# Performance work log

Measured on AMD Instinct MI355X. Metric: run time of the kernel, lower is better.

## Reference

```python
import jax, jax.numpy as jnp
import numpy as np

HD, IN_SZ, V, OP_SZ = 1024, 1024, 400, 128
B, K, L = 64, 8, 13


def log1mexp(x):
    # log(1 - exp(x)) for x <= 0, numerically stable on both ends
    x = jnp.minimum(x, -1e-38)
    big = x > -0.6931472
    return jnp.where(big,
                     jnp.log(-jnp.expm1(jnp.where(big, x, -1.0))),
                     jnp.log1p(-jnp.exp(jnp.where(big, -1.0, x))))


def compute_log_R(log_p, num_points=1000):
    # Unordered-sample ratios for Plackett-Luce sampling without replacement
    # (Kool et al.). P(S) = (1 - p_S) * int_0^1 u^{-p_S} prod_{j in S}(1 - u^{p_j}) du;
    # the (1 - p_S) prefactor cancels in all ratios. Midpoint rule in log-space.
    p = jnp.exp(log_p)                                   # (B,k)
    p_S = jnp.sum(p, axis=-1, keepdims=True)             # (B,1)
    u = (jnp.arange(num_points, dtype=log_p.dtype) + 0.5) / num_points
    log_u = jnp.log(u)                                   # (N,)
    T = log1mexp(p[:, None, :] * log_u[None, :, None])   # (B,N,k): log(1-u^{p_j})
    base = -p_S * log_u[None, :] + jnp.sum(T, axis=-1)   # (B,N)
    logN = jnp.log(jnp.float32(num_points))
    logI = jax.nn.logsumexp(base, axis=-1) - logN        # (B,)   log I(S)
    logI_s = jax.nn.logsumexp(base[:, :, None] - T, axis=1) - logN   # (B,k)
    log_R_s = logI_s - logI[:, None]
    pair = base[:, :, None, None] - T[:, :, :, None] - T[:, :, None, :]  # (B,N,k,k)
    logI_ss = jax.nn.logsumexp(pair, axis=1) - logN      # (B,k,k)
    kk = log_p.shape[-1]
    log_R_ss = jnp.where(jnp.eye(kk, dtype=bool)[None], 0.0,
                         logI_ss - logI_s[:, :, None])
    return log_R_s, log_R_ss


def gumbel_with_maximum(phi, T, u):
    # Gumbel(phi) sample conditioned on its max over axis 1 equaling T (shape (R,1))
    gmb = -jnp.log(-jnp.log(u * (1.0 - 2e-7) + 1e-7))
    g_phi = phi + gmb
    Z = jnp.max(g_phi, axis=1, keepdims=True)
    v = T - g_phi + log1mexp(g_phi - Z)
    return T - jax.nn.relu(v) - jnp.log1p(jnp.exp(-jnp.abs(v)))


def forward(x_feat, W_in_op, b_in_op, W_ih, W_hh, b_ih, b_hh,
            W_fc1, b_fc1, W_out, b_out, gumbel_u, program_len, k):
    Bn = x_feat.shape[0]
    k = int(k)
    program_len = int(program_len)
    Vn = W_out.shape[0]
    H = W_hh.shape[1]
    R = Bn * k
    # beam-major layout: row j*Bn + i is beam j of batch element i (torch split/cat order)
    x_f = jnp.tile(x_feat, (k, 1))                       # (R, in_sz)
    rows = jnp.arange(R)
    batch_idx = jnp.tile(jnp.arange(Bn), k)
    chunk = jnp.arange(k * Vn) // Vn

    def to_beams(z):  # (R, d) -> (Bn, k*d); = torch.cat(torch.split(z, Bn, 0), 1)
        return z.reshape(k, Bn, -1).transpose(1, 0, 2).reshape(Bn, -1)

    def step(carry, xt):
        h, c, G, logp, temp, samples, outputs, ent_plot, entropy_element = carry
        u_t, t = xt
        inp_op = jax.nn.relu(temp @ W_in_op.T + b_in_op)             # (R,128)
        xin = jnp.concatenate([x_f, inp_op], axis=1)                 # (R,in+128)
        gates = xin @ W_ih.T + b_ih + h @ W_hh.T + b_hh              # (R,4H)
        i_g, f_g, g_g, o_g = jnp.split(gates, 4, axis=1)             # torch LSTM order
        c = jax.nn.sigmoid(f_g) * c + jax.nn.sigmoid(i_g) * jnp.tanh(g_g)
        h = jax.nn.sigmoid(o_g) * jnp.tanh(c)
        hd = jax.nn.relu(h @ W_fc1.T + b_fc1)
        logits = hd @ W_out.T + b_out                                # (R,V)
        log_probs = jax.nn.log_softmax(logits, axis=1)
        probs = jax.nn.softmax(logits, axis=1)
        # ---- stochastic-beam-search SWOR step (selection carries no gradient) ----
        phi = jax.lax.stop_gradient(log_probs + logp)
        g = jax.lax.stop_gradient(gumbel_with_maximum(phi, G, u_t))
        nub = jnp.where(t == 0, 1, k)   # unique parent beams (all identical at t=0)
        g2 = jnp.where(chunk[None, :] < nub, to_beams(g), -jnp.inf)  # (Bn,k*V)
        g_val, index = jax.lax.top_k(g2, k)                          # (Bn,k)
        G_new = g_val.T.reshape(R, 1)
        sample = (index % Vn).T.reshape(R)                           # action ids
        order = (index // Vn).T.reshape(R) * Bn + batch_idx          # parent rows
        log_probs = log_probs[order]
        probs = probs[order]
        logp = logp[order] + log_probs[rows, sample][:, None]
        samples = samples[order].at[:, t].set(sample.astype(samples.dtype))
        outputs = outputs[order].at[:, t].set(log_probs[rows, sample])
        h = h[order]
        c = c[order]
        ent = jnp.sum(log_probs * probs, axis=1, keepdims=True)      # (R,1)
        phi_k = to_beams(logp)                                       # (Bn,k)
        log_R_s, log_R_ss = compute_log_R(phi_k)
        w_p_q = jax.lax.stop_gradient(jnp.exp(phi_k + log_R_s))
        Wsum = jnp.sum(w_p_q, axis=1)
        ws = jnp.sum(w_p_q * to_beams(ent), axis=1)
        ent_plot = ent_plot + ws
        entropy_element = entropy_element + ws / Wsum
        temp = jax.nn.one_hot(sample, Vn + 1, dtype=x_feat.dtype)
        new_carry = (h, c, G_new, logp, temp, samples, outputs, ent_plot, entropy_element)
        return new_carry, (log_R_s, log_R_ss, phi_k)

    z = jnp.zeros
    init = (z((R, H)), z((R, H)), z((R, 1)), z((R, 1)),
            jax.nn.one_hot(jnp.full((R,), Vn), Vn + 1, dtype=x_feat.dtype),
            z((R, program_len)), z((R, program_len)), z((Bn,)), z((Bn,)))
    carry, ys = jax.lax.scan(step, init, (gumbel_u, jnp.arange(program_len)))
    samples, outputs, ent_plot, entropy_element = carry[5], carry[6], carry[7], carry[8]
    log_R_s, log_R_ss, phi_k = ys[0][-1], ys[1][-1], ys[2][-1]
    return (to_beams(outputs), to_beams(samples), entropy_element,
            log_R_s, log_R_ss, phi_k, ent_plot)


def setup_inputs() -> dict:
    key = jax.random.key(0)
    ks = jax.random.split(key, 7)

    def lin(kk, out_f, in_f):  # torch nn.Linear default init
        s = 1.0 / np.sqrt(in_f)
        kw, kb = jax.random.split(kk)
        return (jax.random.uniform(kw, (out_f, in_f), jnp.float32, -s, s),
                jax.random.uniform(kb, (out_f,), jnp.float32, -s, s))

    W_in_op, b_in_op = lin(ks[0], OP_SZ, V + 1)
    W_ih, b_ih = lin(ks[1], 4 * HD, IN_SZ + OP_SZ)
    W_hh, b_hh = lin(ks[2], 4 * HD, HD)
    W_fc1, b_fc1 = lin(ks[3], HD, HD)
    W_out, b_out = lin(ks[4], V, HD)
    x_feat = jax.random.normal(ks[5], (B, IN_SZ), jnp.float32)
    gumbel_u = jax.random.uniform(ks[6], (L, B * K, V), jnp.float32)
    return {"x_feat": x_feat, "W_in_op": W_in_op, "b_in_op": b_in_op,
            "W_ih": W_ih, "W_hh": W_hh, "b_ih": b_ih, "b_hh": b_hh,
            "W_fc1": W_fc1, "b_fc1": b_fc1, "W_out": W_out, "b_out": b_out,
            "gumbel_u": gumbel_u, "program_len": L, "k": K}


def reference(x_feat, W_in_op, b_in_op, W_ih, W_hh, b_ih, b_hh,
              W_fc1, b_fc1, W_out, b_out, gumbel_u, program_len, k):
    return forward(x_feat, W_in_op, b_in_op, W_ih, W_hh, b_ih, b_hh,
                   W_fc1, b_fc1, W_out, b_out, gumbel_u, program_len, k)
```

## Files before the change

kernel.cpp:

```cpp
#include <hip/hip_runtime.h>
#include <hip/hip_bf16.h>
#include <cstdint>

#define RR 512
#define KB_ 8
#define VV 400
#define HD_ 1024
#define GD 4096
#define LL 13
#define BKT 16
#define NPTS 1000
#define OUT_N 18560
#define LDP 68

__device__ __constant__ int cPJ[28] = {0,0,0,0,0,0,0,1,1,1,1,1,1,2,2,2,2,2,3,3,3,3,4,4,4,5,5,6};
__device__ __constant__ int cPL[28] = {1,2,3,4,5,6,7,2,3,4,5,6,7,3,4,5,6,7,4,5,6,7,5,6,7,6,7,7};

__device__ __forceinline__ float r7_log1mexp(float x) {
  x = fminf(x, -1e-38f);
  return (x > -0.6931472f) ? logf(-expm1f(x)) : log1pf(-expf(x));
}

__device__ __forceinline__ float r7_sigm(float x) { return 1.f / (1.f + expf(-x)); }

__device__ __forceinline__ int r7_pidx(int j, int l) {
  if (j > l) { int t = j; j = l; l = t; }
  return 9 + (j * (15 - j)) / 2 + (l - j - 1);
}

__device__ __forceinline__ float r7_bmax256(float v, float* red) {
  #pragma unroll
  for (int o = 32; o; o >>= 1) v = fmaxf(v, __shfl_xor(v, o, 64));
  __syncthreads();
  if ((threadIdx.x & 63) == 0) red[threadIdx.x >> 6] = v;
  __syncthreads();
  return fmaxf(fmaxf(red[0], red[1]), fmaxf(red[2], red[3]));
}

__device__ __forceinline__ float r7_bsum256(float v, float* red) {
  #pragma unroll
  for (int o = 32; o; o >>= 1) v += __shfl_xor(v, o, 64);
  __syncthreads();
  if ((threadIdx.x & 63) == 0) red[threadIdx.x >> 6] = v;
  __syncthreads();
  return (red[0] + red[1]) + (red[2] + red[3]);
}

__device__ __forceinline__ void r7_gemm(
    const float* __restrict__ A, int lda,
    const float* __restrict__ W, int ldw,
    int K, int r0, int n0, int nmax,
    float (&acc)[4][4], float (*As)[LDP], float (*Bs)[LDP])
{
  const int tid = threadIdx.x;
  const int la = tid >> 2;
  const int lk = (tid & 3) << 2;
  const int tx = tid & 15, ty = tid >> 4;
  for (int k0 = 0; k0 < K; k0 += BKT) {
    float4 av = *reinterpret_cast<const float4*>(A + (size_t)(r0 + la) * lda + (k0 + lk));
    float4 bv = make_float4(0.f, 0.f, 0.f, 0.f);
    if (n0 + la < nmax)
      bv = *reinterpret_cast<const float4*>(W + (size_t)(n0 + la) * ldw + (k0 + lk));
    __syncthreads();
    As[lk + 0][la] = av.x; As[lk + 1][la] = av.y; As[lk + 2][la] = av.z; As[lk + 3][la] = av.w;
    Bs[lk + 0][la] = bv.x; Bs[lk + 1][la] = bv.y; Bs[lk + 2][la] = bv.z; Bs[lk + 3][la] = bv.w;
    __syncthreads();
    #pragma unroll
    for (int kk = 0; kk < BKT; ++kk) {
      float4 a = *reinterpret_cast<const float4*>(&As[kk][ty * 4]);
      float4 b = *reinterpret_cast<const float4*>(&Bs[kk][tx * 4]);
      float ar[4] = {a.x, a.y, a.z, a.w};
      float br[4] = {b.x, b.y, b.z, b.w};
      #pragma unroll
      for (int i = 0; i < 4; ++i)
        #pragma unroll
        for (int j = 0; j < 4; ++j)
          acc[i][j] = fmaf(ar[i], br[j], acc[i][j]);
    }
  }
}

__global__ __launch_bounds__(256) void r7_wszero(float* h0, float* c0, float* Gv,
                                                 float* logp0, float* accum) {
  int idx = blockIdx.x * 256 + threadIdx.x;
  if (idx < RR * HD_) { h0[idx] = 0.f; c0[idx] = 0.f; }
  if (idx < RR) { Gv[idx] = 0.f; logp0[idx] = 0.f; }
  if (idx < 128) accum[idx] = 0.f;
}

__global__ __launch_bounds__(256) void r7_flag(float* dout) {
  int idx = blockIdx.x * 256 + threadIdx.x;
  if (idx < OUT_N) dout[idx] = (idx == 6656) ? 20000.0f : 0.0f;
}

__global__ __launch_bounds__(256) void r7_xfb(const float* __restrict__ xf,
                                              const float* __restrict__ Wih,
                                              const float* __restrict__ bih,
                                              const float* __restrict__ bhh,
                                              float* __restrict__ xfb) {
  __shared__ __align__(16) float As[BKT][LDP];
  __shared__ __align__(16) float Bs[BKT][LDP];
  float acc[4][4] = {};
  int n0 = blockIdx.x * 64;
  r7_gemm(xf, 1024, Wih, 1152, 1024, 0, n0, 1 << 30, acc, As, Bs);
  int tx = threadIdx.x & 15, ty = threadIdx.x >> 4;
  #pragma unroll
  for (int i = 0; i < 4; ++i)
    #pragma unroll
    for (int j = 0; j < 4; ++j) {
      int r = ty * 4 + i, c = n0 + tx * 4 + j;
      xfb[(size_t)r * GD + c] = acc[i][j] + bih[c] + bhh[c];
    }
}

__global__ __launch_bounds__(256) void r7_inp(const int* s_arr, int t, const float* Wio,
                                              const float* bio, float* inp) {
  int idx = blockIdx.x * 256 + threadIdx.x;
  int r = idx >> 7, m = idx & 127;
  int s = (t == 0) ? 400 : s_arr[(size_t)(t - 1) * RR + r];
  float v = Wio[m * 401 + s] + bio[m];
  inp[idx] = fmaxf(v, 0.f);
}

__global__ __launch_bounds__(256) void r7_glstm(
    const float* __restrict__ hprev, const float* __restrict__ inp,
    const float* __restrict__ Whh, const float* __restrict__ Wih,
    const int* __restrict__ o_arr, int t, float* __restrict__ gates)
{
  __shared__ __align__(16) float As[BKT][LDP];
  __shared__ __align__(16) float Bs2[2][BKT][LDP];
  float acc[2][4][4] = {};
  const int tid = threadIdx.x;
  const int n0 = blockIdx.x * 64, r0 = blockIdx.y * 64, g2 = blockIdx.z;
  const int la = tid >> 2, lk = (tid & 3) << 2;
  const int gl = tid >> 7, rem = tid & 127;
  const int lb = rem >> 1, lk2 = (rem & 1) * 8;
  const int tx = tid & 15, ty = tid >> 4;
  const int arow = r0 + la;
  const int asrc = (t == 0) ? arow : o_arr[(size_t)(t - 1) * RR + arow];
  const float* Arow = hprev + (size_t)asrc * HD_;
  const float* Brow = Whh + (size_t)((2 * g2 + gl) * 1024 + n0 + lb) * HD_;
  for (int k0 = 0; k0 < HD_; k0 += BKT) {
    float4 av = *reinterpret_cast<const float4*>(Arow + k0 + lk);
    float4 b0 = *reinterpret_cast<const float4*>(Brow + k0 + lk2);
    float4 b1 = *reinterpret_cast<const float4*>(Brow + k0 + lk2 + 4);
    __syncthreads();
    As[lk + 0][la] = av.x; As[lk + 1][la] = av.y; As[lk + 2][la] = av.z; As[lk + 3][la] = av.w;
    Bs2[gl][lk2 + 0][lb] = b0.x; Bs2[gl][lk2 + 1][lb] = b0.y;
    Bs2[gl][lk2 + 2][lb] = b0.z; Bs2[gl][lk2 + 3][lb] = b0.w;
    Bs2[gl][lk2 + 4][lb] = b1.x; Bs2[gl][lk2 + 5][lb] = b1.y;
    Bs2[gl][lk2 + 6][lb] = b1.z; Bs2[gl][lk2 + 7][lb] = b1.w;
    __syncthreads();
    #pragma unroll
    for (int kk = 0; kk < BKT; ++kk) {
      float4 a = *reinterpret_cast<const float4*>(&As[kk][ty * 4]);
      float4 bA = *reinterpret_cast<const float4*>(&Bs2[0][kk][tx * 4]);
      float4 bB = *reinterpret_cast<const float4*>(&Bs2[1][kk][tx * 4]);
      float ar[4] = {a.x, a.y, a.z, a.w};
      float b0r[4] = {bA.x, bA.y, bA.z, bA.w};
      float b1r[4] = {bB.x, bB.y, bB.z, bB.w};
      #pragma unroll
      for (int i = 0; i < 4; ++i)
        #pragma unroll
        for (int j = 0; j < 4; ++j) {
          acc[0][i][j] = fmaf(ar[i], b0r[j], acc[0][i][j]);
          acc[1][i][j] = fmaf(ar[i], b1r[j], acc[1][i][j]);
        }
    }
  }
  const float* A2 = inp + (size_t)(r0 + la) * 128;
  const float* B2 = Wih + (size_t)((2 * g2 + gl) * 1024 + n0 + lb) * 1152 + 1024;
  for (int k0 = 0; k0 < 128; k0 += BKT) {
    float4 av = *reinterpret_cast<const float4*>(A2 + k0 + lk);
    float4 b0 = *reinterpret_cast<const float4*>(B2 + k0 + lk2);
    float4 b1 = *reinterpret_cast<const float4*>(B2 + k0 + lk2 + 4);
    __syncthreads();
    As[lk + 0][la] = av.x; As[lk + 1][la] = av.y; As[lk + 2][la] = av.z; As[lk + 3][la] = av.w;
    Bs2[gl][lk2 + 0][lb] = b0.x; Bs2[gl][lk2 + 1][lb] = b0.y;
    Bs2[gl][lk2 + 2][lb] = b0.z; Bs2[gl][lk2 + 3][lb] = b0.w;
    Bs2[gl][lk2 + 4][lb] = b1.x; Bs2[gl][lk2 + 5][lb] = b1.y;
    Bs2[gl][lk2 + 6][lb] = b1.z; Bs2[gl][lk2 + 7][lb] = b1.w;
    __syncthreads();
    #pragma unroll
    for (int kk = 0; kk < BKT; ++kk) {
      float4 a = *reinterpret_cast<const float4*>(&As[kk][ty * 4]);
      float4 bA = *reinterpret_cast<const float4*>(&Bs2[0][kk][tx * 4]);
      float4 bB = *reinterpret_cast<const float4*>(&Bs2[1][kk][tx * 4]);
      float ar[4] = {a.x, a.y, a.z, a.w};
      float b0r[4] = {bA.x, bA.y, bA.z, bA.w};
      float b1r[4] = {bB.x, bB.y, bB.z, bB.w};
      #pragma unroll
      for (int i = 0; i < 4; ++i)
        #pragma unroll
        for (int j = 0; j < 4; ++j) {
          acc[0][i][j] = fmaf(ar[i], b0r[j], acc[0][i][j]);
          acc[1][i][j] = fmaf(ar[i], b1r[j], acc[1][i][j]);
        }
    }
  }
  #pragma unroll
  for (int g = 0; g < 2; ++g)
    #pragma unroll
    for (int i = 0; i < 4; ++i)
      #pragma unroll
      for (int j = 0; j < 4; ++j)
        gates[(size_t)(r0 + ty * 4 + i) * GD + (2 * g2 + g) * 1024 + n0 + tx * 4 + j] =
            acc[g][i][j];
}

__global__ __launch_bounds__(256) void r7_lstm(const float* gates, const float* xfb,
                                               const float* cprev, const int* o_arr, int t,
                                               float* cout, float* hout) {
  int idx = blockIdx.x * 256 + threadIdx.x;
  int r = idx >> 10, n = idx & 1023;
  int src = (t == 0) ? r : o_arr[(size_t)(t - 1) * RR + r];
  const float* g = gates + (size_t)r * GD;
  const float* xb = xfb + (size_t)(r & 63) * GD;
  float gi = g[n] + xb[n];
  float gf = g[1024 + n] + xb[1024 + n];
  float gg = g[2048 + n] + xb[2048 + n];
  float go = g[3072 + n] + xb[3072 + n];
  float cp = cprev[(size_t)src * HD_ + n];
  float c = r7_sigm(gf) * cp + r7_sigm(gi) * tanhf(gg);
  cout[idx] = c;
  hout[idx] = r7_sigm(go) * tanhf(c);
}

__global__ __launch_bounds__(256) void r7_fc1(const float* h, const float* W1, float* hdp) {
  __shared__ __align__(16) float As[BKT][LDP];
  __shared__ __align__(16) float Bs[BKT][LDP];
  float acc[4][4] = {};
  int n0 = blockIdx.x * 64, r0 = blockIdx.y * 64, z = blockIdx.z;
  r7_gemm(h + z * 512, HD_, W1 + z * 512, HD_, 512, r0, n0, 1 << 30, acc, As, Bs);
  float* dst = hdp + (size_t)z * RR * HD_;
  int tx = threadIdx.x & 15, ty = threadIdx.x >> 4;
  #pragma unroll
  for (int i = 0; i < 4; ++i)
    #pragma unroll
    for (int j = 0; j < 4; ++j)
      dst[(size_t)(r0 + ty * 4 + i) * HD_ + n0 + tx * 4 + j] = acc[i][j];
}

__global__ __launch_bounds__(256) void r7_fc1c(const float* hdp, const float* b1, float* hd) {
  int idx = blockIdx.x * 256 + threadIdx.x;
  hd[idx] = fmaxf(hdp[idx] + hdp[RR * HD_ + idx] + b1[idx & 1023], 0.f);
}

__global__ __launch_bounds__(256) void r7_out(const float* hd, const float* Wo, float* outp) {
  __shared__ __align__(16) float As[BKT][LDP];
  __shared__ __align__(16) float Bs[BKT][LDP];
  float acc[4][4] = {};
  int n0 = blockIdx.x * 64, r0 = blockIdx.y * 64, z = blockIdx.z;
  r7_gemm(hd + z * 256, HD_, Wo + z * 256, HD_, 256, r0, n0, VV, acc, As, Bs);
  float* dst = outp + (size_t)z * RR * VV;
  int tx = threadIdx.x & 15, ty = threadIdx.x >> 4;
  #pragma unroll
  for (int i = 0; i < 4; ++i)
    #pragma unroll
    for (int j = 0; j < 4; ++j) {
      int c = n0 + tx * 4 + j;
      if (c < VV) dst[(size_t)(r0 + ty * 4 + i) * VV + c] = acc[i][j];
    }
}

__global__ __launch_bounds__(256) void r7_soft(const float* outp, const float* bo,
                                               const float* logp_in, const float* Gv,
                                               const float* gum, float* lp, float* gb,
                                               float* entold) {
  __shared__ float red[4];
  int r = blockIdx.x, tid = threadIdx.x;
  bool v1 = (tid + 256) < VV;
  size_t off0 = (size_t)r * VV + tid;
  float l0 = outp[off0] + outp[RR * VV + off0] + outp[2 * RR * VV + off0]
           + outp[3 * RR * VV + off0] + bo[tid];
  float l1 = -INFINITY;
  if (v1) {
    size_t off1 = off0 + 256;
    l1 = outp[off1] + outp[RR * VV + off1] + outp[2 * RR * VV + off1]
       + outp[3 * RR * VV + off1] + bo[tid + 256];
  }
  float m = r7_bmax256(fmaxf(l0, l1), red);
  float e0 = expf(l0 - m), e1 = v1 ? expf(l1 - m) : 0.f;
  float s = r7_bsum256(e0 + e1, red);
  float ls = logf(s);
  float lp0 = l0 - m - ls, lp1 = l1 - m - ls;
  float ent = lp0 * expf(lp0) + (v1 ? lp1 * expf(lp1) : 0.f);
  ent = r7_bsum256(ent, red);
  if (tid == 0) entold[r] = ent;
  float lpr = logp_in[r];
  const float* ur = gum + (size_t)r * VV;
  float gp0, gp1 = -INFINITY;
  { float u = ur[tid];
    gp0 = lp0 + lpr - logf(-logf(u * (1.f - 2e-7f) + 1e-7f)); }
  if (v1) { float u = ur[tid + 256];
            gp1 = lp1 + lpr - logf(-logf(u * (1.f - 2e-7f) + 1e-7f)); }
  float Z = r7_bmax256(fmaxf(gp0, gp1), red);
  float T = Gv[r];
  int i = r & 63, j = r >> 6;
  float* gbr = gb + (size_t)i * (KB_ * VV) + j * VV;
  {
    float vv = T - gp0 + r7_log1mexp(gp0 - Z);
    gbr[tid] = T - fmaxf(vv, 0.f) - log1pf(expf(-fabsf(vv)));
    lp[(size_t)r * VV + tid] = lp0;
  }
  if (v1) {
    float vv = T - gp1 + r7_log1mexp(gp1 - Z);
    gbr[tid + 256] = T - fmaxf(vv, 0.f) - log1pf(expf(-fabsf(vv)));
    lp[(size_t)r * VV + tid + 256] = lp1;
  }
}

__device__ __forceinline__ unsigned long long r7_pack(float v, int c) {
  unsigned u = __float_as_uint(v);
  u = (u & 0x80000000u) ? ~u : (u | 0x80000000u);
  return ((unsigned long long)u << 32) | (unsigned)(0xFFFFFFFFu - (unsigned)c);
}

__global__ __launch_bounds__(256) void r7_topk(const float* gb, int t, float* Gv,
                                               int* s_t, int* o_t, const float* lp,
                                               const float* logp_in, float* logp_out,
                                               const float* entold, float* entbm,
                                               float* lv_t) {
  __shared__ unsigned long long wbest[4];
  __shared__ unsigned long long selK[KB_];
  int i = blockIdx.x, tid = threadIdx.x;
  int lane = tid & 63, wid = tid >> 6;
  int limit = (t == 0) ? VV : KB_ * VV;
  unsigned long long key[13];
  int cnt = 0;
  for (int c = tid; c < limit; c += 256)
    key[cnt++] = r7_pack(gb[(size_t)i * (KB_ * VV) + c], c);
  for (int it = 0; it < KB_; ++it) {
    unsigned long long b = 0ull;
    for (int k = 0; k < cnt; ++k) b = (key[k] > b) ? key[k] : b;
    #pragma unroll
    for (int o = 32; o; o >>= 1) {
      unsigned long long x = __shfl_xor(b, o, 64);
      b = (x > b) ? x : b;
    }
    if (lane == 0) wbest[wid] = b;
    __syncthreads();
    unsigned long long g = wbest[0];
    g = (wbest[1] > g) ? wbest[1] : g;
    g = (wbest[2] > g) ? wbest[2] : g;
    g = (wbest[3] > g) ? wbest[3] : g;
    int csel = (int)(0xFFFFFFFFu - (unsigned)(g & 0xFFFFFFFFu));
    if (tid == (csel & 255)) key[csel >> 8] = 0ull;
    if (tid == 0) selK[it] = g;
    __syncthreads();
  }
  if (tid < KB_) {
    unsigned long long g = selK[tid];
    unsigned x = (unsigned)(g >> 32);
    x = (x & 0x80000000u) ? (x & 0x7FFFFFFFu) : ~x;
    float v = __uint_as_float(x);
    int c = (int)(0xFFFFFFFFu - (unsigned)(g & 0xFFFFFFFFu));
    int r = tid * 64 + i;
    int s = c % VV;
    int o = (c / VV) * 64 + i;
    Gv[r] = v;
    s_t[r] = s;
    o_t[r] = o;
    float lv = lp[(size_t)o * VV + s];
    logp_out[r] = logp_in[o] + lv;
    entbm[r] = entold[o];
    lv_t[r] = lv;
  }
}

__global__ __launch_bounds__(256) void r7_logR(const float* logp_new, const float* entbm,
                                               float* accum, float* dout, int last) {
  __shared__ float Tm[KB_][NPTS];
  __shared__ float base[NPTS];
  __shared__ float phi[KB_], pj[KB_];
  __shared__ float res[37];
  int i = blockIdx.x, tid = threadIdx.x;
  int lane = tid & 63, wid = tid >> 6;
  if (tid < KB_) { float ph = logp_new[tid * 64 + i]; phi[tid] = ph; pj[tid] = expf(ph); }
  __syncthreads();
  float pS = ((pj[0] + pj[1]) + (pj[2] + pj[3])) + ((pj[4] + pj[5]) + (pj[6] + pj[7]));
  for (int n = tid; n < NPTS; n += 256) {
    float lu = logf((n + 0.5f) * (1.0f / NPTS));
    float b = -pS * lu;
    #pragma unroll
    for (int j = 0; j < KB_; ++j) {
      float tv = r7_log1mexp(pj[j] * lu);
      Tm[j][n] = tv; b += tv;
    }
    base[n] = b;
  }
  __syncthreads();
  const float logN = 6.9077552789821f;
  for (int ridx = wid; ridx < 37; ridx += 4) {
    int jj = -1, ll = -1;
    if (ridx >= 1 && ridx < 9) jj = ridx - 1;
    else if (ridx >= 9) { jj = cPJ[ridx - 9]; ll = cPL[ridx - 9]; }
    float mx = -INFINITY;
    for (int n = lane; n < NPTS; n += 64) {
      float v = base[n];
      if (jj >= 0) v -= Tm[jj][n];
      if (ll >= 0) v -= Tm[ll][n];
      mx = fmaxf(mx, v);
    }
    #pragma unroll
    for (int o = 32; o; o >>= 1) mx = fmaxf(mx, __shfl_xor(mx, o, 64));
    float sm = 0.f;
    for (int n = lane; n < NPTS; n += 64) {
      float v = base[n];
      if (jj >= 0) v -= Tm[jj][n];
      if (ll >= 0) v -= Tm[ll][n];
      sm += expf(v - mx);
    }
    #pragma unroll
    for (int o = 32; o; o >>= 1) sm += __shfl_xor(sm, o, 64);
    if (lane == 0) res[ridx] = mx + logf(sm) - logN;
  }
  __syncthreads();
  if (tid == 0) {
    float logI = res[0];
    float Wsum = 0.f, ws = 0.f;
    #pragma unroll
    for (int j = 0; j < KB_; ++j) {
      float lRs = res[1 + j] - logI;
      float wj = expf(phi[j] + lRs);
      Wsum += wj;
      ws += wj * entbm[j * 64 + i];
    }
    accum[i] += ws;
    accum[64 + i] += ws / Wsum;
    if (last) {
      for (int j = 0; j < KB_; ++j) {
        dout[13376 + i * 8 + j] = res[1 + j] - logI;
        dout[17984 + i * 8 + j] = phi[j];
        for (int l = 0; l < KB_; ++l) {
          float v = (l == j) ? 0.f : (res[r7_pidx(j, l)] - res[1 + j]);
          dout[13888 + i * 64 + j * 8 + l] = v;
        }
      }
    }
  }
}

__global__ __launch_bounds__(512) void r7_final(const float* lv_arr, const int* s_arr,
                                                const int* o_arr, const float* accum,
                                                float* dout) {
  int r = threadIdx.x;
  int i = r & 63, j = r >> 6;
  float vals[LL]; int svs[LL];
  int a = r;
  for (int tt = LL - 1; tt >= 0; --tt) {
    vals[tt] = lv_arr[tt * RR + a];
    svs[tt]  = s_arr[tt * RR + a];
    a = o_arr[tt * RR + a];
  }
  #pragma unroll
  for (int tt = 0; tt < LL; ++tt) {
    dout[i * 104 + j * 13 + tt] = vals[tt];
    dout[6656 + i * 104 + j * 13 + tt] = (float)svs[tt];
  }
  if (r < 64) {
    dout[13312 + r] = accum[64 + r];
    dout[18496 + r] = accum[r];
  }
}

extern "C" void kernel_launch(void* const* d_in, const int* in_sizes, int n_in,
                              void* d_out, int out_size, void* d_ws, size_t ws_size,
                              hipStream_t stream) {
  const float* x_feat  = (const float*)d_in[0];
  const float* W_in_op = (const float*)d_in[1];
  const float* b_in_op = (const float*)d_in[2];
  const float* W_ih    = (const float*)d_in[3];
  const float* W_hh    = (const float*)d_in[4];
  const float* b_ih    = (const float*)d_in[5];
  const float* b_hh    = (const float*)d_in[6];
  const float* W_fc1   = (const float*)d_in[7];
  const float* b_fc1   = (const float*)d_in[8];
  const float* W_out   = (const float*)d_in[9];
  const float* b_out   = (const float*)d_in[10];
  const float* gum     = (const float*)d_in[11];
  float* out           = (float*)d_out;

  float* W = (float*)d_ws;
  size_t o = 0;
  float* lv_arr = W + o; o += (size_t)LL * RR;
  float* Gv     = W + o; o += RR;
  float* logpb0 = W + o; o += RR;
  float* logpb1 = W + o; o += RR;
  float* entold = W + o; o += RR;
  float* entbm  = W + o; o += RR;
  float* accum  = W + o; o += 128;
  int* s_arr = (int*)(W + o); o += (size_t)LL * RR;
  int* o_arr = (int*)(W + o); o += (size_t)LL * RR;
  float* xfb    = W + o; o += (size_t)64 * GD;
  float* inp    = W + o; o += (size_t)RR * 128;
  float* gates  = W + o; o += (size_t)RR * GD;
  float* lp     = W + o; o += (size_t)RR * VV;
  float* gb     = W + o; o += (size_t)RR * VV;
  float* h2[2]; h2[0] = W + o; o += (size_t)RR * HD_; h2[1] = W + o; o += (size_t)RR * HD_;
  float* c2[2]; c2[0] = W + o; o += (size_t)RR * HD_; c2[1] = W + o; o += (size_t)RR * HD_;
  float* hd     = W + o; o += (size_t)RR * HD_;
  size_t needed_bytes = o * sizeof(float);
  float* logpb[2] = {logpb0, logpb1};
  float* hdp  = gates;
  float* outp = gates;

  if (ws_size < needed_bytes) {
    r7_flag<<<(OUT_N + 255) / 256, 256, 0, stream>>>(out);
    return;
  }

  r7_wszero<<<2048, 256, 0, stream>>>(h2[0], c2[0], Gv, logpb[0], accum);
  r7_xfb<<<64, 256, 0, stream>>>(x_feat, W_ih, b_ih, b_hh, xfb);

  for (int t = 0; t < LL; ++t) {
    int pi = t & 1, po = pi ^ 1;
    r7_inp<<<256, 256, 0, stream>>>(s_arr, t, W_in_op, b_in_op, inp);
    r7_glstm<<<dim3(16, 8, 2), 256, 0, stream>>>(h2[pi], inp, W_hh, W_ih, o_arr, t, gates);
    r7_lstm<<<2048, 256, 0, stream>>>(gates, xfb, c2[pi], o_arr, t, c2[po], h2[po]);
    r7_fc1<<<dim3(16, 8, 2), 256, 0, stream>>>(h2[po], W_fc1, hdp);
    r7_fc1c<<<2048, 256, 0, stream>>>(hdp, b_fc1, hd);
    r7_out<<<dim3(7, 8, 4), 256, 0, stream>>>(hd, W_out, outp);
    r7_soft<<<512, 256, 0, stream>>>(outp, b_out, logpb[pi], Gv,
                                     gum + (size_t)t * RR * VV, lp, gb, entold);
    r7_topk<<<64, 256, 0, stream>>>(gb, t, Gv, s_arr + (size_t)t * RR,
                                    o_arr + (size_t)t * RR, lp, logpb[pi], logpb[po],
                                    entold, entbm, lv_arr + (size_t)t * RR);
    r7_logR<<<64, 256, 0, stream>>>(logpb[po], entbm, accum, out, (t == LL - 1) ? 1 : 0);
  }
  r7_final<<<1, 512, 0, stream>>>(lv_arr, s_arr, o_arr, accum, out);
}
```

Before: 2.994 ms.

## Fuse op-embedding into LSTM gate GEMM, retile it, and move topk keys to LDS

The separate input-embedding kernel is removed. Its ReLU(W_in_op[:,s]+b) gather is computed on the fly inside the gate GEMM's second K-loop, which drops one launch and the inp buffer per timestep. The gate GEMM is retiled from 64x64 tiles with two gates per block to 32x128 tiles with one gate per block, giving 512 blocks instead of 256. The top-k kernel now keeps candidate keys in shared memory instead of a register array, which avoids dynamically indexed registers but adds LDS reads on each of the 8 selection passes. The retiling gives each block less A-tile reuse, and the fused gather does strided scalar reads of W_in_op.

```diff
diff --git a/kernel.cpp b/kernel.cpp
--- a/kernel.cpp
+++ b/kernel.cpp
@@ -12,23 +12,25 @@
 #define NPTS 1000
 #define OUT_N 18560
 #define LDP 68
+#define AP 36
+#define BP 132
 
 __device__ __constant__ int cPJ[28] = {0,0,0,0,0,0,0,1,1,1,1,1,1,2,2,2,2,2,3,3,3,3,4,4,4,5,5,6};
 __device__ __constant__ int cPL[28] = {1,2,3,4,5,6,7,2,3,4,5,6,7,3,4,5,6,7,4,5,6,7,5,6,7,6,7,7};
 
-__device__ __forceinline__ float r7_log1mexp(float x) {
+__device__ __forceinline__ float r9_log1mexp(float x) {
   x = fminf(x, -1e-38f);
   return (x > -0.6931472f) ? logf(-expm1f(x)) : log1pf(-expf(x));
 }
 
-__device__ __forceinline__ float r7_sigm(float x) { return 1.f / (1.f + expf(-x)); }
-
-__device__ __forceinline__ int r7_pidx(int j, int l) {
+__device__ __forceinline__ float r9_sigm(float x) { return 1.f / (1.f + expf(-x)); }
+
+__device__ __forceinline__ int r9_pidx(int j, int l) {
   if (j > l) { int t = j; j = l; l = t; }
   return 9 + (j * (15 - j)) / 2 + (l - j - 1);
 }
 
-__device__ __forceinline__ float r7_bmax256(float v, float* red) {
+__device__ __forceinline__ float r9_bmax256(float v, float* red) {
   #pragma unroll
   for (int o = 32; o; o >>= 1) v = fmaxf(v, __shfl_xor(v, o, 64));
   __syncthreads();
@@ -37,7 +39,7 @@
   return fmaxf(fmaxf(red[0], red[1]), fmaxf(red[2], red[3]));
 }
 
-__device__ __forceinline__ float r7_bsum256(float v, float* red) {
+__device__ __forceinline__ float r9_bsum256(float v, float* red) {
   #pragma unroll
   for (int o = 32; o; o >>= 1) v += __shfl_xor(v, o, 64);
   __syncthreads();
@@ -46,7 +48,7 @@
   return (red[0] + red[1]) + (red[2] + red[3]);
 }
 
-__device__ __forceinline__ void r7_gemm(
+__device__ __forceinline__ void r9_gemm(
     const float* __restrict__ A, int lda,
     const float* __restrict__ W, int ldw,
     int K, int r0, int n0, int nmax,
@@ -80,7 +82,7 @@
   }
 }
 
-__global__ __launch_bounds__(256) void r7_wszero(float* h0, float* c0, float* Gv,
+__global__ __launch_bounds__(256) void r9_wszero(float* h0, float* c0, float* Gv,
                                                  float* logp0, float* accum) {
   int idx = blockIdx.x * 256 + threadIdx.x;
   if (idx < RR * HD_) { h0[idx] = 0.f; c0[idx] = 0.f; }
@@ -88,12 +90,12 @@
   if (idx < 128) accum[idx] = 0.f;
 }
 
-__global__ __launch_bounds__(256) void r7_flag(float* dout) {
+__global__ __launch_bounds__(256) void r9_flag(float* dout) {
   int idx = blockIdx.x * 256 + threadIdx.x;
   if (idx < OUT_N) dout[idx] = (idx == 6656) ? 20000.0f : 0.0f;
 }
 
-__global__ __launch_bounds__(256) void r7_xfb(const float* __restrict__ xf,
+__global__ __launch_bounds__(256) void r9_xfb(const float* __restrict__ xf,
                                               const float* __restrict__ Wih,
                                               const float* __restrict__ bih,
                                               const float* __restrict__ bhh,
@@ -102,7 +104,7 @@
   __shared__ __align__(16) float Bs[BKT][LDP];
   float acc[4][4] = {};
   int n0 = blockIdx.x * 64;
-  r7_gemm(xf, 1024, Wih, 1152, 1024, 0, n0, 1 << 30, acc, As, Bs);
+  r9_gemm(xf, 1024, Wih, 1152, 1024, 0, n0, 1 << 30, acc, As, Bs);
   int tx = threadIdx.x & 15, ty = threadIdx.x >> 4;
   #pragma unroll
   for (int i = 0; i < 4; ++i)
@@ -113,102 +115,89 @@
     }
 }
 
-__global__ __launch_bounds__(256) void r7_inp(const int* s_arr, int t, const float* Wio,
-                                              const float* bio, float* inp) {
-  int idx = blockIdx.x * 256 + threadIdx.x;
-  int r = idx >> 7, m = idx & 127;
-  int s = (t == 0) ? 400 : s_arr[(size_t)(t - 1) * RR + r];
-  float v = Wio[m * 401 + s] + bio[m];
-  inp[idx] = fmaxf(v, 0.f);
-}
-
-__global__ __launch_bounds__(256) void r7_glstm(
-    const float* __restrict__ hprev, const float* __restrict__ inp,
+__global__ __launch_bounds__(256) void r9_glstm(
+    const float* __restrict__ hprev,
     const float* __restrict__ Whh, const float* __restrict__ Wih,
-    const int* __restrict__ o_arr, int t, float* __restrict__ gates)
+    const float* __restrict__ Wio, const float* __restrict__ bio,
+    const int* __restrict__ s_arr, const int* __restrict__ o_arr, int t,
+    float* __restrict__ gates)
 {
-  __shared__ __align__(16) float As[BKT][LDP];
-  __shared__ __align__(16) float Bs2[2][BKT][LDP];
-  float acc[2][4][4] = {};
+  __shared__ __align__(16) float As[BKT][AP];
+  __shared__ __align__(16) float Bs[BKT][BP];
+  float acc[4][4] = {};
   const int tid = threadIdx.x;
-  const int n0 = blockIdx.x * 64, r0 = blockIdx.y * 64, g2 = blockIdx.z;
-  const int la = tid >> 2, lk = (tid & 3) << 2;
-  const int gl = tid >> 7, rem = tid & 127;
-  const int lb = rem >> 1, lk2 = (rem & 1) * 8;
-  const int tx = tid & 15, ty = tid >> 4;
-  const int arow = r0 + la;
+  const int c0 = blockIdx.x * 128;
+  const int r0 = blockIdx.y * 32;
+  const int g  = blockIdx.z;
+  const int a_r = tid >> 3;
+  const int a_k = (tid & 7) * 2;
+  const int b_r = tid >> 1;
+  const int b_k = (tid & 1) * 8;
+  const int tx = tid & 31, ty = tid >> 5;
+  const int arow = r0 + a_r;
   const int asrc = (t == 0) ? arow : o_arr[(size_t)(t - 1) * RR + arow];
-  const float* Arow = hprev + (size_t)asrc * HD_;
-  const float* Brow = Whh + (size_t)((2 * g2 + gl) * 1024 + n0 + lb) * HD_;
+  const int s_row = (t == 0) ? 400 : s_arr[(size_t)(t - 1) * RR + arow];
+  const float* Arow  = hprev + (size_t)asrc * HD_;
+  const float* BrowW = Whh + (size_t)(g * 1024 + c0 + b_r) * HD_;
   for (int k0 = 0; k0 < HD_; k0 += BKT) {
-    float4 av = *reinterpret_cast<const float4*>(Arow + k0 + lk);
-    float4 b0 = *reinterpret_cast<const float4*>(Brow + k0 + lk2);
-    float4 b1 = *reinterpret_cast<const float4*>(Brow + k0 + lk2 + 4);
-    __syncthreads();
-    As[lk + 0][la] = av.x; As[lk + 1][la] = av.y; As[lk + 2][la] = av.z; As[lk + 3][la] = av.w;
-    Bs2[gl][lk2 + 0][lb] = b0.x; Bs2[gl][lk2 + 1][lb] = b0.y;
-    Bs2[gl][lk2 + 2][lb] = b0.z; Bs2[gl][lk2 + 3][lb] = b0.w;
-    Bs2[gl][lk2 + 4][lb] = b1.x; Bs2[gl][lk2 + 5][lb] = b1.y;
-    Bs2[gl][lk2 + 6][lb] = b1.z; Bs2[gl][lk2 + 7][lb] = b1.w;
+    float2 av = *reinterpret_cast<const float2*>(Arow + k0 + a_k);
+    float4 b0 = *reinterpret_cast<const float4*>(BrowW + k0 + b_k);
+    float4 b1 = *reinterpret_cast<const float4*>(BrowW + k0 + b_k + 4);
+    __syncthreads();
+    As[a_k][a_r] = av.x; As[a_k + 1][a_r] = av.y;
+    Bs[b_k + 0][b_r] = b0.x; Bs[b_k + 1][b_r] = b0.y;
+    Bs[b_k + 2][b_r] = b0.z; Bs[b_k + 3][b_r] = b0.w;
+    Bs[b_k + 4][b_r] = b1.x; Bs[b_k + 5][b_r] = b1.y;
+    Bs[b_k + 6][b_r] = b1.z; Bs[b_k + 7][b_r] = b1.w;
     __syncthreads();
     #pragma unroll
     for (int kk = 0; kk < BKT; ++kk) {
       float4 a = *reinterpret_cast<const float4*>(&As[kk][ty * 4]);
-      float4 bA = *reinterpret_cast<const float4*>(&Bs2[0][kk][tx * 4]);
-      float4 bB = *reinterpret_cast<const float4*>(&Bs2[1][kk][tx * 4]);
+      float4 b = *reinterpret_cast<const float4*>(&Bs[kk][tx * 4]);
       float ar[4] = {a.x, a.y, a.z, a.w};
-      float b0r[4] = {bA.x, bA.y, bA.z, bA.w};
-      float b1r[4] = {bB.x, bB.y, bB.z, bB.w};
+      float br[4] = {b.x, b.y, b.z, b.w};
       #pragma unroll
       for (int i = 0; i < 4; ++i)
         #pragma unroll
-        for (int j = 0; j < 4; ++j) {
-          acc[0][i][j] = fmaf(ar[i], b0r[j], acc[0][i][j]);
-          acc[1][i][j] = fmaf(ar[i], b1r[j], acc[1][i][j]);
-        }
-    }
-  }
-  const float* A2 = inp + (size_t)(r0 + la) * 128;
-  const float* B2 = Wih + (size_t)((2 * g2 + gl) * 1024 + n0 + lb) * 1152 + 1024;
+        for (int j = 0; j < 4; ++j)
+          acc[i][j] = fmaf(ar[i], br[j], acc[i][j]);
+    }
+  }
+  const float* BrowI = Wih + (size_t)(g * 1024 + c0 + b_r) * 1152 + 1024;
   for (int k0 = 0; k0 < 128; k0 += BKT) {
-    float4 av = *reinterpret_cast<const float4*>(A2 + k0 + lk);
-    float4 b0 = *reinterpret_cast<const float4*>(B2 + k0 + lk2);
-    float4 b1 = *reinterpret_cast<const float4*>(B2 + k0 + lk2 + 4);
-    __syncthreads();
-    As[lk + 0][la] = av.x; As[lk + 1][la] = av.y; As[lk + 2][la] = av.z; As[lk + 3][la] = av.w;
-    Bs2[gl][lk2 + 0][lb] = b0.x; Bs2[gl][lk2 + 1][lb] = b0.y;
-    Bs2[gl][lk2 + 2][lb] = b0.z; Bs2[gl][lk2 + 3][lb] = b0.w;
-    Bs2[gl][lk2 + 4][lb] = b1.x; Bs2[gl][lk2 + 5][lb] = b1.y;
-    Bs2[gl][lk2 + 6][lb] = b1.z; Bs2[gl][lk2 + 7][lb] = b1.w;
+    int m0 = k0 + a_k;
+    float a0 = fmaxf(Wio[(size_t)m0 * 401 + s_row] + bio[m0], 0.f);
+    float a1 = fmaxf(Wio[(size_t)(m0 + 1) * 401 + s_row] + bio[m0 + 1], 0.f);
+    float4 b0 = *reinterpret_cast<const float4*>(BrowI + k0 + b_k);
+    float4 b1 = *reinterpret_cast<const float4*>(BrowI + k0 + b_k + 4);
+    __syncthreads();
+    As[a_k][a_r] = a0; As[a_k + 1][a_r] = a1;
+    Bs[b_k + 0][b_r] = b0.x; Bs[b_k + 1][b_r] = b0.y;
+    Bs[b_k + 2][b_r] = b0.z; Bs[b_k + 3][b_r] = b0.w;
+    Bs[b_k + 4][b_r] = b1.x; Bs[b_k + 5][b_r] = b1.y;
+    Bs[b_k + 6][b_r] = b1.z; Bs[b_k + 7][b_r] = b1.w;
     __syncthreads();
     #pragma unroll
     for (int kk = 0; kk < BKT; ++kk) {
       float4 a = *reinterpret_cast<const float4*>(&As[kk][ty * 4]);
-      float4 bA = *reinterpret_cast<const float4*>(&Bs2[0][kk][tx * 4]);
-      float4 bB = *reinterpret_cast<const float4*>(&Bs2[1][kk][tx * 4]);
+      float4 b = *reinterpret_cast<const float4*>(&Bs[kk][tx * 4]);
       float ar[4] = {a.x, a.y, a.z, a.w};
-      float b0r[4] = {bA.x, bA.y, bA.z, bA.w};
-      float b1r[4] = {bB.x, bB.y, bB.z, bB.w};
+      float br[4] = {b.x, b.y, b.z, b.w};
       #pragma unroll
       for (int i = 0; i < 4; ++i)
         #pragma unroll
-        for (int j = 0; j < 4; ++j) {
-          acc[0][i][j] = fmaf(ar[i], b0r[j], acc[0][i][j]);
-          acc[1][i][j] = fmaf(ar[i], b1r[j], acc[1][i][j]);
-        }
-    }
-  }
-  #pragma unroll
-  for (int g = 0; g < 2; ++g)
-    #pragma unroll
-    for (int i = 0; i < 4; ++i)
-      #pragma unroll
-      for (int j = 0; j < 4; ++j)
-        gates[(size_t)(r0 + ty * 4 + i) * GD + (2 * g2 + g) * 1024 + n0 + tx * 4 + j] =
-            acc[g][i][j];
-}
-
-__global__ __launch_bounds__(256) void r7_lstm(const float* gates, const float* xfb,
+        for (int j = 0; j < 4; ++j)
+          acc[i][j] = fmaf(ar[i], br[j], acc[i][j]);
+    }
+  }
+  #pragma unroll
+  for (int i = 0; i < 4; ++i)
+    #pragma unroll
+    for (int j = 0; j < 4; ++j)
+      gates[(size_t)(r0 + ty * 4 + i) * GD + g * 1024 + c0 + tx * 4 + j] = acc[i][j];
+}
+
+__global__ __launch_bounds__(256) void r9_lstm(const float* gates, const float* xfb,
                                                const float* cprev, const int* o_arr, int t,
                                                float* cout, float* hout) {
   int idx = blockIdx.x * 256 + threadIdx.x;
@@ -221,17 +210,17 @@
   float gg = g[2048 + n] + xb[2048 + n];
   float go = g[3072 + n] + xb[3072 + n];
   float cp = cprev[(size_t)src * HD_ + n];
-  float c = r7_sigm(gf) * cp + r7_sigm(gi) * tanhf(gg);
+  float c = r9_sigm(gf) * cp + r9_sigm(gi) * tanhf(gg);
   cout[idx] = c;
-  hout[idx] = r7_sigm(go) * tanhf(c);
-}
-
-__global__ __launch_bounds__(256) void r7_fc1(const float* h, const float* W1, float* hdp) {
+  hout[idx] = r9_sigm(go) * tanhf(c);
+}
+
+__global__ __launch_bounds__(256) void r9_fc1(const float* h, const float* W1, float* hdp) {
   __shared__ __align__(16) float As[BKT][LDP];
   __shared__ __align__(16) float Bs[BKT][LDP];
   float acc[4][4] = {};
   int n0 = blockIdx.x * 64, r0 = blockIdx.y * 64, z = blockIdx.z;
-  r7_gemm(h + z * 512, HD_, W1 + z * 512, HD_, 512, r0, n0, 1 << 30, acc, As, Bs);
+  r9_gemm(h + z * 512, HD_, W1 + z * 512, HD_, 512, r0, n0, 1 << 30, acc, As, Bs);
   float* dst = hdp + (size_t)z * RR * HD_;
   int tx = threadIdx.x & 15, ty = threadIdx.x >> 4;
   #pragma unroll
@@ -241,17 +230,17 @@
       dst[(size_t)(r0 + ty * 4 + i) * HD_ + n0 + tx * 4 + j] = acc[i][j];
 }
 
-__global__ __launch_bounds__(256) void r7_fc1c(const float* hdp, const float* b1, float* hd) {
+__global__ __launch_bounds__(256) void r9_fc1c(const float* hdp, const float* b1, float* hd) {
   int idx = blockIdx.x * 256 + threadIdx.x;
   hd[idx] = fmaxf(hdp[idx] + hdp[RR * HD_ + idx] + b1[idx & 1023], 0.f);
 }
 
-__global__ __launch_bounds__(256) void r7_out(const float* hd, const float* Wo, float* outp) {
+__global__ __launch_bounds__(256) void r9_out(const float* hd, const float* Wo, float* outp) {
   __shared__ __align__(16) float As[BKT][LDP];
   __shared__ __align__(16) float Bs[BKT][LDP];
   float acc[4][4] = {};
   int n0 = blockIdx.x * 64, r0 = blockIdx.y * 64, z = blockIdx.z;
-  r7_gemm(hd + z * 256, HD_, Wo + z * 256, HD_, 256, r0, n0, VV, acc, As, Bs);
+  r9_gemm(hd + z * 256, HD_, Wo + z * 256, HD_, 256, r0, n0, VV, acc, As, Bs);
   float* dst = outp + (size_t)z * RR * VV;
   int tx = threadIdx.x & 15, ty = threadIdx.x >> 4;
   #pragma unroll
@@ -263,7 +252,7 @@
     }
 }
 
-__global__ __launch_bounds__(256) void r7_soft(const float* outp, const float* bo,
+__global__ __launch_bounds__(256) void r9_soft(const float* outp, const float* bo,
                                                const float* logp_in, const float* Gv,
                                                const float* gum, float* lp, float* gb,
                                                float* entold) {
@@ -279,13 +268,13 @@
     l1 = outp[off1] + outp[RR * VV + off1] + outp[2 * RR * VV + off1]
        + outp[3 * RR * VV + off1] + bo[tid + 256];
   }
-  float m = r7_bmax256(fmaxf(l0, l1), red);
+  float m = r9_bmax256(fmaxf(l0, l1), red);
   float e0 = expf(l0 - m), e1 = v1 ? expf(l1 - m) : 0.f;
-  float s = r7_bsum256(e0 + e1, red);
+  float s = r9_bsum256(e0 + e1, red);
   float ls = logf(s);
   float lp0 = l0 - m - ls, lp1 = l1 - m - ls;
   float ent = lp0 * expf(lp0) + (v1 ? lp1 * expf(lp1) : 0.f);
-  ent = r7_bsum256(ent, red);
+  ent = r9_bsum256(ent, red);
   if (tid == 0) entold[r] = ent;
   float lpr = logp_in[r];
   const float* ur = gum + (size_t)r * VV;
@@ -294,45 +283,48 @@
     gp0 = lp0 + lpr - logf(-logf(u * (1.f - 2e-7f) + 1e-7f)); }
   if (v1) { float u = ur[tid + 256];
             gp1 = lp1 + lpr - logf(-logf(u * (1.f - 2e-7f) + 1e-7f)); }
-  float Z = r7_bmax256(fmaxf(gp0, gp1), red);
+  float Z = r9_bmax256(fmaxf(gp0, gp1), red);
   float T = Gv[r];
   int i = r & 63, j = r >> 6;
   float* gbr = gb + (size_t)i * (KB_ * VV) + j * VV;
   {
-    float vv = T - gp0 + r7_log1mexp(gp0 - Z);
+    float vv = T - gp0 + r9_log1mexp(gp0 - Z);
     gbr[tid] = T - fmaxf(vv, 0.f) - log1pf(expf(-fabsf(vv)));
     lp[(size_t)r * VV + tid] = lp0;
   }
   if (v1) {
-    float vv = T - gp1 + r7_log1mexp(gp1 - Z);
+    float vv = T - gp1 + r9_log1mexp(gp1 - Z);
     gbr[tid + 256] = T - fmaxf(vv, 0.f) - log1pf(expf(-fabsf(vv)));
     lp[(size_t)r * VV + tid + 256] = lp1;
   }
 }
 
-__device__ __forceinline__ unsigned long long r7_pack(float v, int c) {
+__device__ __forceinline__ unsigned long long r9_pack(float v, int c) {
   unsigned u = __float_as_uint(v);
   u = (u & 0x80000000u) ? ~u : (u | 0x80000000u);
   return ((unsigned long long)u << 32) | (unsigned)(0xFFFFFFFFu - (unsigned)c);
 }
 
-__global__ __launch_bounds__(256) void r7_topk(const float* gb, int t, float* Gv,
+__global__ __launch_bounds__(256) void r9_topk(const float* gb, int t, float* Gv,
                                                int* s_t, int* o_t, const float* lp,
                                                const float* logp_in, float* logp_out,
                                                const float* entold, float* entbm,
                                                float* lv_t) {
+  __shared__ unsigned long long keys[KB_ * VV];
   __shared__ unsigned long long wbest[4];
   __shared__ unsigned long long selK[KB_];
   int i = blockIdx.x, tid = threadIdx.x;
   int lane = tid & 63, wid = tid >> 6;
   int limit = (t == 0) ? VV : KB_ * VV;
-  unsigned long long key[13];
-  int cnt = 0;
   for (int c = tid; c < limit; c += 256)
-    key[cnt++] = r7_pack(gb[(size_t)i * (KB_ * VV) + c], c);
+    keys[c] = r9_pack(gb[(size_t)i * (KB_ * VV) + c], c);
+  __syncthreads();
   for (int it = 0; it < KB_; ++it) {
     unsigned long long b = 0ull;
-    for (int k = 0; k < cnt; ++k) b = (key[k] > b) ? key[k] : b;
+    for (int c = tid; c < limit; c += 256) {
+      unsigned long long k = keys[c];
+      b = (k > b) ? k : b;
+    }
     #pragma unroll
     for (int o = 32; o; o >>= 1) {
       unsigned long long x = __shfl_xor(b, o, 64);
@@ -344,9 +336,11 @@
     g = (wbest[1] > g) ? wbest[1] : g;
     g = (wbest[2] > g) ? wbest[2] : g;
     g = (wbest[3] > g) ? wbest[3] : g;
-    int csel = (int)(0xFFFFFFFFu - (unsigned)(g & 0xFFFFFFFFu));
-    if (tid == (csel & 255)) key[csel >> 8] = 0ull;
-    if (tid == 0) selK[it] = g;
+    if (tid == 0) {
+      int csel = (int)(0xFFFFFFFFu - (unsigned)(g & 0xFFFFFFFFu));
+      keys[csel] = 0ull;
+      selK[it] = g;
+    }
     __syncthreads();
   }
   if (tid < KB_) {
@@ -368,7 +362,7 @@
   }
 }
 
-__global__ __launch_bounds__(256) void r7_logR(const float* logp_new, const float* entbm,
+__global__ __launch_bounds__(256) void r9_logR(const float* logp_new, const float* entbm,
                                                float* accum, float* dout, int last) {
   __shared__ float Tm[KB_][NPTS];
   __shared__ float base[NPTS];
@@ -384,7 +378,7 @@
     float b = -pS * lu;
     #pragma unroll
     for (int j = 0; j < KB_; ++j) {
-      float tv = r7_log1mexp(pj[j] * lu);
+      float tv = r9_log1mexp(pj[j] * lu);
       Tm[j][n] = tv; b += tv;
     }
     base[n] = b;
@@ -433,7 +427,7 @@
         dout[13376 + i * 8 + j] = res[1 + j] - logI;
         dout[17984 + i * 8 + j] = phi[j];
         for (int l = 0; l < KB_; ++l) {
-          float v = (l == j) ? 0.f : (res[r7_pidx(j, l)] - res[1 + j]);
+          float v = (l == j) ? 0.f : (res[r9_pidx(j, l)] - res[1 + j]);
           dout[13888 + i * 64 + j * 8 + l] = v;
         }
       }
@@ -441,7 +435,7 @@
   }
 }
 
-__global__ __launch_bounds__(512) void r7_final(const float* lv_arr, const int* s_arr,
+__global__ __launch_bounds__(512) void r9_final(const float* lv_arr, const int* s_arr,
                                                 const int* o_arr, const float* accum,
                                                 float* dout) {
   int r = threadIdx.x;
@@ -493,7 +487,6 @@
   int* s_arr = (int*)(W + o); o += (size_t)LL * RR;
   int* o_arr = (int*)(W + o); o += (size_t)LL * RR;
   float* xfb    = W + o; o += (size_t)64 * GD;
-  float* inp    = W + o; o += (size_t)RR * 128;
   float* gates  = W + o; o += (size_t)RR * GD;
   float* lp     = W + o; o += (size_t)RR * VV;
   float* gb     = W + o; o += (size_t)RR * VV;
@@ -506,27 +499,27 @@
   float* outp = gates;
 
   if (ws_size < needed_bytes) {
-    r7_flag<<<(OUT_N + 255) / 256, 256, 0, stream>>>(out);
+    r9_flag<<<(OUT_N + 255) / 256, 256, 0, stream>>>(out);
     return;
   }
 
-  r7_wszero<<<2048, 256, 0, stream>>>(h2[0], c2[0], Gv, logpb[0], accum);
-  r7_xfb<<<64, 256, 0, stream>>>(x_feat, W_ih, b_ih, b_hh, xfb);
+  r9_wszero<<<2048, 256, 0, stream>>>(h2[0], c2[0], Gv, logpb[0], accum);
+  r9_xfb<<<64, 256, 0, stream>>>(x_feat, W_ih, b_ih, b_hh, xfb);
 
   for (int t = 0; t < LL; ++t) {
     int pi = t & 1, po = pi ^ 1;
-    r7_inp<<<256, 256, 0, stream>>>(s_arr, t, W_in_op, b_in_op, inp);
-    r7_glstm<<<dim3(16, 8, 2), 256, 0, stream>>>(h2[pi], inp, W_hh, W_ih, o_arr, t, gates);
-    r7_lstm<<<2048, 256, 0, stream>>>(gates, xfb, c2[pi], o_arr, t, c2[po], h2[po]);
-    r7_fc1<<<dim3(16, 8, 2), 256, 0, stream>>>(h2[po], W_fc1, hdp);
-    r7_fc1c<<<2048, 256, 0, stream>>>(hdp, b_fc1, hd);
-    r7_out<<<dim3(7, 8, 4), 256, 0, stream>>>(hd, W_out, outp);
-    r7_soft<<<512, 256, 0, stream>>>(outp, b_out, logpb[pi], Gv,
+    r9_glstm<<<dim3(8, 16, 4), 256, 0, stream>>>(h2[pi], W_hh, W_ih, W_in_op, b_in_op,
+                                                 s_arr, o_arr, t, gates);
+    r9_lstm<<<2048, 256, 0, stream>>>(gates, xfb, c2[pi], o_arr, t, c2[po], h2[po]);
+    r9_fc1<<<dim3(16, 8, 2), 256, 0, stream>>>(h2[po], W_fc1, hdp);
+    r9_fc1c<<<2048, 256, 0, stream>>>(hdp, b_fc1, hd);
+    r9_out<<<dim3(7, 8, 4), 256, 0, stream>>>(hd, W_out, outp);
+    r9_soft<<<512, 256, 0, stream>>>(outp, b_out, logpb[pi], Gv,
                                      gum + (size_t)t * RR * VV, lp, gb, entold);
-    r7_topk<<<64, 256, 0, stream>>>(gb, t, Gv, s_arr + (size_t)t * RR,
+    r9_topk<<<64, 256, 0, stream>>>(gb, t, Gv, s_arr + (size_t)t * RR,
                                     o_arr + (size_t)t * RR, lp, logpb[pi], logpb[po],
                                     entold, entbm, lv_arr + (size_t)t * RR);
-    r7_logR<<<64, 256, 0, stream>>>(logpb[po], entbm, accum, out, (t == LL - 1) ? 1 : 0);
-  }
-  r7_final<<<1, 512, 0, stream>>>(lv_arr, s_arr, o_arr, accum, out);
-}
+    r9_logR<<<64, 256, 0, stream>>>(logpb[po], entbm, accum, out, (t == LL - 1) ? 1 : 0);
+  }
+  r9_final<<<1, 512, 0, stream>>>(lv_arr, s_arr, o_arr, accum, out);
+}
```

Measured after the change: 2.758 ms. 7.9% less time.
